# Kernel optimization log

Hardware: AMD Instinct MI355X
Metric: run time of the kernel (lower is better)

Reference implementation:

```python
import jax, jax.numpy as jnp
import numpy as np

B, S = 64, 100
N_EX, N_Q = 3000, 128
N_AT, N_IT = 1000, 1000
D_A = D_E = D_K = 128
GAMMA = 0.03


def _xavier(k, shape):
    lim = float(np.sqrt(6.0 / (shape[0] + shape[1])))
    return jax.random.uniform(k, shape, jnp.float32, -lim, lim)


def setup_inputs() -> dict:
    key = jax.random.key(0)
    ks = jax.random.split(key, 20)
    nq1 = N_Q + 1
    e_data = jax.random.randint(ks[0], (B, S), 0, N_EX, dtype=jnp.int32)
    a_data = jax.random.randint(ks[1], (B, S), 0, 2, dtype=jnp.int32)
    it_data = jax.random.randint(ks[2], (B, S), 0, N_IT, dtype=jnp.int32)
    at_data = jax.random.randint(ks[3], (B, S), 0, N_AT, dtype=jnp.int32)
    # binary Q-matrix with zeros replaced by gamma (as done in LPKT.__init__)
    q_bin = (jax.random.uniform(ks[4], (N_EX + 10, nq1)) < 0.05).astype(jnp.float32)
    q_matrix = jnp.where(q_bin > 0, 1.0, GAMMA)
    E_at = _xavier(ks[5], (N_AT + 10, D_K))
    E_it = _xavier(ks[6], (N_IT + 10, D_K))
    E_e = _xavier(ks[7], (N_EX + 10, D_E))
    h0 = _xavier(ks[8], (nq1, D_K))  # xavier-initialized initial skill state
    W1 = _xavier(ks[9], (D_A + D_E + D_K, D_K)); b1 = jnp.zeros(D_K, jnp.float32)
    W2 = _xavier(ks[10], (4 * D_K, D_K)); b2 = jnp.zeros(D_K, jnp.float32)
    W3 = _xavier(ks[11], (4 * D_K, D_K)); b3 = jnp.zeros(D_K, jnp.float32)
    W4 = _xavier(ks[12], (3 * D_K, D_K)); b4 = jnp.zeros(D_K, jnp.float32)
    W5 = _xavier(ks[13], (D_E + D_K, D_K)); b5 = jnp.zeros(D_K, jnp.float32)
    return dict(e_data=e_data, a_data=a_data, it_data=it_data, at_data=at_data,
                q_matrix=q_matrix, h0=h0, E_e=E_e, E_at=E_at, E_it=E_it,
                W1=W1, b1=b1, W2=W2, b2=b2, W3=W3, b3=b3, W4=W4, b4=b4, W5=W5, b5=b5)


def reference(e_data, a_data, it_data, at_data, q_matrix, h0, E_e, E_at, E_it,
              W1, b1, W2, b2, W3, b3, W4, b4, W5, b5):
    Bv, Sv = e_data.shape
    d_k = W2.shape[1]
    d_a = W1.shape[0] - E_e.shape[1] - d_k
    e_emb = E_e[e_data]            # (B,S,d_e)
    at_emb = E_at[at_data]         # (B,S,d_k)
    it_emb = E_it[it_data]         # (B,S,d_k)
    a_rep = jnp.broadcast_to(a_data.astype(jnp.float32)[..., None], (Bv, Sv, d_a))
    all_learning = jnp.concatenate([e_emb, at_emb, a_rep], 2) @ W1 + b1  # (B,S,d_k)
    q_all = q_matrix[e_data]       # (B,S,nq1)
    h_pre0 = jnp.broadcast_to(h0, (Bv,) + h0.shape)  # (B,nq1,d_k)
    q0 = q_all[:, 0]
    ht0 = jnp.einsum('bn,bnd->bd', q0, h_pre0) / q0.sum(1, keepdims=True)
    W4h, W4l, W4i = jnp.split(W4, 3, axis=0)

    def step(carry, x):
        learning_pre, h_pre, h_tilde_pre = carry
        q_e, q_next, it, learning, e_next = x
        feat = jnp.concatenate([learning_pre, it, learning, h_tilde_pre], 1)  # (B,4dk)
        lg = jnp.tanh(feat @ W2 + b2)
        gamma_l = jax.nn.sigmoid(feat @ W3 + b3)
        LG = gamma_l * (lg + 1.0) * 0.5                       # (B,d_k)
        LG_tilde = q_e[:, :, None] * LG[:, None, :]           # (B,nq1,d_k); dropout=eval identity
        gamma_f = jax.nn.sigmoid(jnp.einsum('bnd,df->bnf', h_pre, W4h)
                                 + (LG @ W4l + it @ W4i + b4)[:, None, :])
        h = LG_tilde + gamma_f * h_pre
        h_tilde = jnp.einsum('bn,bnd->bd', q_next, h) / q_next.sum(1, keepdims=True)
        y = jax.nn.sigmoid(jnp.concatenate([e_next, h_tilde], 1) @ W5 + b5).sum(1) / d_k
        return (learning, h, h_tilde), y

    xs = (jnp.swapaxes(q_all[:, :-1], 0, 1), jnp.swapaxes(q_all[:, 1:], 0, 1),
          jnp.swapaxes(it_emb[:, :-1], 0, 1), jnp.swapaxes(all_learning[:, :-1], 0, 1),
          jnp.swapaxes(e_emb[:, 1:], 0, 1))
    learning_pre0 = jnp.zeros((Bv, d_k), jnp.float32)
    _, ys = jax.lax.scan(step, (learning_pre0, h_pre0, ht0), xs)  # ys: (S-1,B)
    pred = jnp.zeros((Bv, Sv), jnp.float32).at[:, 1:].set(ys.T)
    return pred
```

## Files before the change

### kernel.cpp

```cpp
#include <hip/hip_runtime.h>
#include <hip/hip_fp16.h>
#include <math.h>


#define BB   64
#define SS   100
#define DK   128
#define NTH  512

#define OFF_PW1AB   0
#define OFF_PW23ABC 16384
#define OFF_PW4I    65536
#define OFF_PW5A    73728
#define OFF_PW23D   81920
#define OFF_PW4L    98304
#define OFF_PW5B    106496
#define OFF_AFRAG   114688
#define OFF_S1      122880
#define OFF_AL      123008
#define OFF_PRE     532608
#define OFF_HTV     2171008

typedef __attribute__((ext_vector_type(16))) float floatx16;
typedef __attribute__((ext_vector_type(8)))  short short8v;

__device__ __forceinline__ float frcp(float x) { return __builtin_amdgcn_rcpf(x); }
__device__ __forceinline__ float fsig(float x) { float t = __expf(-x); return frcp(1.0f + t); }
__device__ __forceinline__ float ftanh(float x) {
    x = fminf(20.0f, fmaxf(-20.0f, x));
    float t = __expf(-2.0f * x);
    return (1.0f - t) * frcp(1.0f + t);
}
__device__ __forceinline__ float rlf(float v, int s) {
    return __int_as_float(__builtin_amdgcn_readlane(__float_as_int(v), s));
}
__device__ __forceinline__ unsigned bfbits(float x) {
    unsigned u = __float_as_uint(x);
    return (u + 0x7fffu + ((u >> 16) & 1u)) >> 16;
}
__device__ __forceinline__ unsigned pack2(float a, float b) {
    return bfbits(a) | (bfbits(b) << 16);
}
__device__ __forceinline__ float blo(unsigned u) { return __uint_as_float(u << 16); }
__device__ __forceinline__ float bhi(unsigned u) { return __uint_as_float(u & 0xffff0000u); }

__device__ __forceinline__ void wg_barrier() {
    asm volatile("s_waitcnt lgkmcnt(0)" ::: "memory");
    __builtin_amdgcn_s_barrier();
    asm volatile("" ::: "memory");
}

__global__ void k0_prep(const float* __restrict__ W1, const float* __restrict__ W2,
                        const float* __restrict__ W3, const float* __restrict__ W4,
                        const float* __restrict__ W5, unsigned* __restrict__ ws) {
    int g = blockIdx.x * blockDim.x + threadIdx.x;
    if (g < 16384) {
        int s = g >> 7, d = g & 127;
        ws[OFF_PW1AB + g] = pack2(W1[(2*s)*DK + d], W1[(2*s+1)*DK + d]);
    } else if (g < 65536) {
        int i = g - 16384; int s = i >> 8, j = i & 255;
        const float* M = (j < 128) ? W2 : W3; int jj = j & 127;
        ws[g] = pack2(M[(2*s)*DK + jj], M[(2*s+1)*DK + jj]);
    } else if (g < 73728) {
        int i = g - 65536; int s = i >> 7, j = i & 127;
        ws[g] = pack2(W4[(256+2*s)*DK + j], W4[(257+2*s)*DK + j]);
    } else if (g < 81920) {
        int i = g - 73728; int s = i >> 7, j = i & 127;
        ws[g] = pack2(W5[(2*s)*DK + j], W5[(2*s+1)*DK + j]);
    } else if (g < 98304) {
        int i = g - 81920; int s = i & 31, j = (i >> 5) & 255, kh = i >> 13;
        int k0 = 64*kh + 2*s;
        const float* M = (j < 128) ? W2 : W3; int jj = j & 127;
        ws[g] = pack2(M[(384+k0)*DK + jj], M[(385+k0)*DK + jj]);
    } else if (g < 106496) {
        int i = g - 98304; int s = i & 15, j = (i >> 4) & 127, kq = i >> 11;
        int k0 = 32*kq + 2*s;
        ws[g] = pack2(W4[(128+k0)*DK + j], W4[(129+k0)*DK + j]);
    } else if (g < 114688) {
        int i = g - 106496; int s = i & 15, j = (i >> 4) & 127, kq = i >> 11;
        int k0 = 32*kq + 2*s;
        ws[g] = pack2(W5[(128+k0)*DK + j], W5[(129+k0)*DK + j]);
    } else if (g < 122880) {
        int i = g - 114688;
        int gg = i >> 11, kb = (i >> 8) & 7, ln = (i >> 2) & 63, c = i & 3;
        int m = ln & 31, hp = ln >> 5;
        int k0 = 16*kb + 8*hp + 2*c;
        ws[g] = pack2(W4[k0*DK + 32*gg + m], W4[(k0+1)*DK + 32*gg + m]);
    } else if (g < 123008) {
        int d = g - 122880;
        float z = 0.f;
        for (int k = 0; k < 128; k++) z += W1[(256+k)*DK + d];
        ws[g] = __float_as_uint(z);
    }
}

__global__ __launch_bounds__(128)
void k1_al(const int* __restrict__ e_data, const int* __restrict__ a_data,
           const int* __restrict__ at_data, const float* __restrict__ Ee,
           const float* __restrict__ Eat, const float* __restrict__ b1,
           unsigned* __restrict__ ws) {
    const int b = blockIdx.x, t0 = 4 * blockIdx.y, tid = threadIdx.x;
    __shared__ __align__(16) float s_f[4][256];
    #pragma unroll
    for (int r = 0; r < 8; r++) {
        int id = r * 128 + tid; int i = id >> 8, k = id & 255;
        int t = t0 + i; float v = 0.f;
        if (t <= 98) {
            int e  = e_data[b*SS + t];
            int at = at_data[b*SS + t];
            v = (k < 128) ? Ee[(size_t)e*DK + k] : Eat[(size_t)at*DK + (k-128)];
        }
        s_f[i][k] = v;
    }
    __syncthreads();
    float s1v = __uint_as_float(ws[OFF_S1 + tid]);
    float b1v = b1[tid];
    float z[4];
    #pragma unroll
    for (int i = 0; i < 4; i++) z[i] = 0.f;
    #pragma unroll 2
    for (int s = 0; s < 128; s++) {
        unsigned w = ws[OFF_PW1AB + s*128 + tid];
        float wl = blo(w), wh = bhi(w);
        #pragma unroll
        for (int i = 0; i < 4; i++) {
            float2 f = *(const float2*)&s_f[i][2*s];
            z[i] += f.x*wl + f.y*wh;
        }
    }
    __half* AL = (__half*)(ws + OFF_AL);
    #pragma unroll
    for (int i = 0; i < 4; i++) {
        int t = t0 + i;
        if (t <= 98) {
            float a = (float)a_data[b*SS + t];
            AL[(size_t)(b*SS + t)*DK + tid] = __float2half(z[i] + a*s1v + b1v);
        }
    }
}

__global__ __launch_bounds__(512)
void k2_pre(const int* __restrict__ e_data, const int* __restrict__ it_data,
            const float* __restrict__ Eit, const float* __restrict__ Ee,
            const float* __restrict__ b2, const float* __restrict__ b3,
            const float* __restrict__ b4, const float* __restrict__ b5,
            unsigned* __restrict__ ws) {
    const int b = blockIdx.x, t0 = 4 * blockIdx.y, tid = threadIdx.x;
    __shared__ __align__(16) float s_g[4][384];
    __shared__ __align__(16) float s_e[4][128];
    const __half* AL = (const __half*)(ws + OFF_AL);
    #pragma unroll
    for (int r = 0; r < 3; r++) {
        int id = r * 512 + tid; int i = id / 384; int k = id - 384*i;
        int t = t0 + i; float v = 0.f;
        if (t <= 98) {
            if (k < 128)      v = (t == 0) ? 0.f : (float)AL[(size_t)(b*SS + t - 1)*DK + k];
            else if (k < 256) v = Eit[(size_t)it_data[b*SS + t]*DK + (k - 128)];
            else              v = (float)AL[(size_t)(b*SS + t)*DK + (k - 256)];
        }
        s_g[i][k] = v;
    }
    {
        int id = tid; int i = id >> 7, k = id & 127;
        int t = t0 + i;
        s_e[i][k] = (t <= 98) ? Ee[(size_t)e_data[b*SS + t + 1]*DK + k] : 0.f;
    }
    __syncthreads();
    __half* PRE = (__half*)(ws + OFF_PRE);
    float z[4];
    #pragma unroll
    for (int i = 0; i < 4; i++) z[i] = 0.f;
    int col; float bb;
    if (tid < 256) {
        int j = tid;
        #pragma unroll 2
        for (int s = 0; s < 192; s++) {
            unsigned w = ws[OFF_PW23ABC + s*256 + j];
            float wl = blo(w), wh = bhi(w);
            #pragma unroll
            for (int i = 0; i < 4; i++) {
                float2 f = *(const float2*)&s_g[i][2*s];
                z[i] += f.x*wl + f.y*wh;
            }
        }
        col = j; bb = (j < 128) ? b2[j] : b3[j - 128];
    } else if (tid < 384) {
        int j = tid - 256;
        #pragma unroll 2
        for (int s = 0; s < 64; s++) {
            unsigned w = ws[OFF_PW4I + s*128 + j];
            float wl = blo(w), wh = bhi(w);
            #pragma unroll
            for (int i = 0; i < 4; i++) {
                float2 f = *(const float2*)&s_g[i][128 + 2*s];
                z[i] += f.x*wl + f.y*wh;
            }
        }
        col = 256 + j; bb = b4[j];
    } else {
        int j = tid - 384;
        #pragma unroll 2
        for (int s = 0; s < 64; s++) {
            unsigned w = ws[OFF_PW5A + s*128 + j];
            float wl = blo(w), wh = bhi(w);
            #pragma unroll
            for (int i = 0; i < 4; i++) {
                float2 f = *(const float2*)&s_e[i][2*s];
                z[i] += f.x*wl + f.y*wh;
            }
        }
        col = 384 + j; bb = b5[j];
    }
    #pragma unroll
    for (int i = 0; i < 4; i++) {
        int t = t0 + i;
        if (t <= 98) PRE[(size_t)(b*SS + t)*512 + col] = __float2half(z[i] + bb);
    }
}

__global__ __launch_bounds__(NTH, 2)
void lpkt_kernel(const int* __restrict__ e_data, const float* __restrict__ qm,
                 const float* __restrict__ h0, unsigned* __restrict__ ws)
{
    const int b    = blockIdx.x;
    const int tid  = threadIdx.x;
    const int lane = tid & 63;
    const int w    = tid >> 6;
    const int g    = w & 3;
    const int hh   = w >> 2;
    const int h5   = lane >> 5;
    const int l31  = lane & 31;
    const int j1   = tid & 255;
    const int kq4  = w & 3;
    const int j4   = ((w >> 2) << 6) + lane;

    __shared__ __align__(16) unsigned s_frag[8192];
    __shared__ __align__(16) float s_big[2 * 128 * 34];
    __shared__ __align__(16) float s_pre[2][512];
    __shared__ __align__(16) float s_htv[128];
    __shared__ __align__(16) float s_LG[128];
    __shared__ __align__(16) float s_h128[128];
    __shared__ __align__(16) float s_c[128];
    __shared__ __align__(16) float s_l128[2][128];
    __shared__ __align__(16) float s_red[512];
    __shared__ __align__(16) float s_redE[512];
    __shared__ __align__(16) float s_q[3][160];
    __shared__ int   s_ed[100];
    __shared__ float s_scal[1];

    uint4    afru[8];
    unsigned w23[32], w4l[16];
    float    hreg[2][16];

    #pragma unroll
    for (int kb = 0; kb < 8; kb++)
        afru[kb] = ((const uint4*)(ws + OFF_AFRAG))[g*512 + kb*64 + lane];
    #pragma unroll
    for (int s = 0; s < 32; s++) w23[s] = ws[OFF_PW23D + ((hh*256 + j1) << 5) + s];
    #pragma unroll
    for (int s = 0; s < 16; s++) w4l[s] = ws[OFF_PW4L + ((kq4*128 + j4) << 4) + s];

    const __half* PRE = (const __half*)(ws + OFF_PRE);
    __half*       HTV = (__half*)(ws + OFF_HTV);

    if (tid < 100) s_ed[tid] = e_data[b*SS + tid];
    if (tid < 160) { s_q[0][tid] = 0.f; s_q[1][tid] = 0.f; s_q[2][tid] = 0.f; }
    if (tid < 129) {
        s_q[0][tid] = qm[(size_t)e_data[b*SS + 0]*129 + tid];
        s_q[1][tid] = qm[(size_t)e_data[b*SS + 1]*129 + tid];
    }
    s_pre[0][tid] = __half2float(PRE[(size_t)(b*SS)*512 + tid]);
    float  q_pf   = (tid < 129) ? qm[(size_t)e_data[b*SS + 2]*129 + tid] : 0.f;
    __half pre_pf = PRE[(size_t)(b*SS + 1)*512 + tid];

    #pragma unroll
    for (int i = 0; i < 2; i++) {
        const int cb = 2*hh + i;
        const int n = 32*cb + l31;
        #pragma unroll
        for (int r = 0; r < 16; r++) {
            int d = 32*g + (r&3) + 8*(r>>2) + 4*h5;
            hreg[i][r] = h0[(size_t)n*DK + d];
        }
        #pragma unroll
        for (int q = 0; q < 4; q++) {
            int kb = 2*g + (q>>1);
            int lanep = l31 + ((q&1) << 5);
            int off = (((kb*4 + cb) << 10) + lanep*16 + (h5 << 3)) >> 2;
            uint2 pr = make_uint2(pack2(hreg[i][4*q],   hreg[i][4*q+1]),
                                  pack2(hreg[i][4*q+2], hreg[i][4*q+3]));
            *(uint2*)(s_frag + off) = pr;
        }
    }
    if (tid < 128) s_h128[tid] = h0[(size_t)128*DK + tid];
    __syncthreads();
    {
        if (w == 7) {
            float v = s_q[0][lane] + s_q[0][64+lane] + ((lane < 32) ? s_q[0][128+lane] : 0.f);
            #pragma unroll
            for (int m = 32; m > 0; m >>= 1) v += __shfl_xor(v, m);
            if (lane == 0) s_scal[0] = v;
        }
        float vv0[16];
        #pragma unroll
        for (int i = 0; i < 2; i++) {
            float qv = s_q[0][32*(2*hh + i) + l31];
            #pragma unroll
            for (int r = 0; r < 16; r++) {
                float p = qv * hreg[i][r];
                vv0[r] = i ? (vv0[r] + p) : p;
            }
        }
        #pragma unroll
        for (int r = 0; r < 16; r++) {
            int d = 32*g + (r&3) + 8*(r>>2) + 4*h5;
            s_big[(hh*128 + d)*34 + l31] = vv0[r];
        }
    }
    __syncthreads();
    if (tid < 128) {
        float a0 = 0.f, a1 = 0.f;
        #pragma unroll
        for (int jj = 0; jj < 16; jj++) {
            float2 x = *(const float2*)&s_big[tid*34 + 2*jj];
            float2 y = *(const float2*)&s_big[(128 + tid)*34 + 2*jj];
            a0 += x.x + x.y; a1 += y.x + y.y;
        }
        s_htv[tid] = (a0 + a1 + s_q[0][128]*s_h128[tid]) * frcp(s_scal[0]);
    }
    __syncthreads();

    for (int t = 0; t < SS - 1; t++) {
        const int pbp = t & 1;
        const float* qc = s_q[t % 3];
        const float* qn = s_q[(t + 1) % 3];

        if (t + 2 <= 99 && tid < 129) s_q[(t + 2) % 3][tid] = q_pf;
        if (t + 1 <= 98)              s_pre[1 - pbp][tid] = __half2float(pre_pf);
        if (t + 3 <= 99 && tid < 129) q_pf  = qm[(size_t)s_ed[t + 3]*129 + tid];
        if (t + 2 <= 98)              pre_pf = PRE[(size_t)(b*SS + t + 2)*512 + tid];
        if (w == 7) {
            float v = qn[lane] + qn[64 + lane] + ((lane < 32) ? qn[128 + lane] : 0.f);
            #pragma unroll
            for (int m = 32; m > 0; m >>= 1) v += __shfl_xor(v, m);
            if (lane == 0) s_scal[0] = v;
        }
        floatx16 am[2];
        #pragma unroll
        for (int i = 0; i < 2; i++) {
            const int cb = 2*hh + i;
            floatx16 a = (floatx16)(0.f);
            #pragma unroll
            for (int kb = 0; kb < 8; kb++) {
                short8v bf = *(const short8v*)((const char*)s_frag +
                               (((kb*4 + cb) << 10) + lane*16));
                a = __builtin_amdgcn_mfma_f32_32x32x16_bf16(
                        __builtin_bit_cast(short8v, afru[kb]), bf, a, 0, 0, 0);
            }
            am[i] = a;
        }
        {
            float part = 0.f;
            #pragma unroll
            for (int kbl = 0; kbl < 4; kbl++) {
                const int kb = 4*hh + kbl;
                const int kb0 = 16*kb + 8*h5;
                uint4 u = afru[kb];
                part += s_h128[kb0+0]*blo(u.x) + s_h128[kb0+1]*bhi(u.x);
                part += s_h128[kb0+2]*blo(u.y) + s_h128[kb0+3]*bhi(u.y);
                part += s_h128[kb0+4]*blo(u.z) + s_h128[kb0+5]*bhi(u.z);
                part += s_h128[kb0+6]*blo(u.w) + s_h128[kb0+7]*bhi(u.w);
            }
            part += __shfl_xor(part, 32);
            if (h5 == 0) s_l128[hh][32*g + l31] = part;
        }
        {
            float4 fv = ((const float4*)s_htv)[(hh << 4) + (l31 & 15)];
            float z0 = 0.f, z1 = 0.f, z2 = 0.f, z3 = 0.f;
            #pragma unroll
            for (int s = 0; s < 16; s++) {
                float a0 = rlf(fv.x, s), a1 = rlf(fv.y, s);
                float a2 = rlf(fv.z, s), a3 = rlf(fv.w, s);
                unsigned wA = w23[2*s], wB = w23[2*s+1];
                z0 += a0*blo(wA);  z1 += a1*bhi(wA);
                z2 += a2*blo(wB);  z3 += a3*bhi(wB);
            }
            s_red[(hh << 8) + j1] = (z0 + z1) + (z2 + z3);
        }
        wg_barrier();
        {
            const int m = 32*kq4 + l31;
            float z2v = s_red[m]       + s_red[256 + m] + s_pre[pbp][m];
            float z3v = s_red[128 + m] + s_red[384 + m] + s_pre[pbp][128 + m];
            float LGv = fsig(z3v) * (ftanh(z2v) + 1.f) * 0.5f;
            if (w < 4 && h5 == 0) s_LG[m] = LGv;
            float z0 = 0.f, z1 = 0.f, z2 = 0.f, z3 = 0.f;
            #pragma unroll
            for (int s = 0; s < 8; s++) {
                unsigned wA = w4l[2*s], wB = w4l[2*s+1];
                float a0 = rlf(LGv, 4*s+0), a1 = rlf(LGv, 4*s+1);
                float a2 = rlf(LGv, 4*s+2), a3 = rlf(LGv, 4*s+3);
                z0 += a0*blo(wA);  z1 += a1*bhi(wA);
                z2 += a2*blo(wB);  z3 += a3*bhi(wB);
            }
            s_redE[(kq4 << 7) + j4] = (z0 + z1) + (z2 + z3);
        }
        wg_barrier();
        if (tid < 128)
            s_c[tid] = s_redE[tid] + s_redE[128+tid] + s_redE[256+tid] + s_redE[384+tid]
                     + s_pre[pbp][256 + tid];
        wg_barrier();
        {
            float lgv[16], cvv[16], vv[16];
            const float4* LG4 = (const float4*)s_LG;
            const float4* C4  = (const float4*)s_c;
            #pragma unroll
            for (int u = 0; u < 4; u++) {
                float4 lg = LG4[8*g + 2*u + h5];
                float4 cc = C4 [8*g + 2*u + h5];
                lgv[4*u+0]=lg.x; lgv[4*u+1]=lg.y; lgv[4*u+2]=lg.z; lgv[4*u+3]=lg.w;
                cvv[4*u+0]=cc.x; cvv[4*u+1]=cc.y; cvv[4*u+2]=cc.z; cvv[4*u+3]=cc.w;
            }
            #pragma unroll
            for (int i = 0; i < 2; i++) {
                const int cb = 2*hh + i;
                const int n = 32*cb + l31;
                const float qcv = qc[n], qnv = qn[n];
                #pragma unroll
                for (int r = 0; r < 16; r++) {
                    float gg = fsig(am[i][r] + cvv[r]);
                    float hn = qcv*lgv[r] + gg*hreg[i][r];
                    hreg[i][r] = hn;
                    float p = qnv*hn;
                    vv[r] = i ? (vv[r] + p) : p;
                }
            }
            #pragma unroll
            for (int i = 0; i < 2; i++) {
                const int cb = 2*hh + i;
                #pragma unroll
                for (int q = 0; q < 4; q++) {
                    int kb = 2*g + (q>>1);
                    int lanep = l31 + ((q&1) << 5);
                    int off = (((kb*4 + cb) << 10) + lanep*16 + (h5 << 3)) >> 2;
                    uint2 pr = make_uint2(pack2(hreg[i][4*q],   hreg[i][4*q+1]),
                                          pack2(hreg[i][4*q+2], hreg[i][4*q+3]));
                    *(uint2*)(s_frag + off) = pr;
                }
            }
            #pragma unroll
            for (int r = 0; r < 16; r++) {
                int d = 32*g + (r&3) + 8*(r>>2) + 4*h5;
                s_big[(hh*128 + d)*34 + l31] = vv[r];
            }
            if (tid < 128) {
                float gg = fsig(s_l128[0][tid] + s_l128[1][tid] + s_c[tid]);
                s_h128[tid] = qc[128]*s_LG[tid] + gg*s_h128[tid];
            }
        }
        wg_barrier();
        if (tid < 128) {
            float a0 = 0.f, a1 = 0.f;
            #pragma unroll
            for (int jj = 0; jj < 16; jj++) {
                float2 x = *(const float2*)&s_big[tid*34 + 2*jj];
                float2 y = *(const float2*)&s_big[(128 + tid)*34 + 2*jj];
                a0 += x.x + x.y; a1 += y.x + y.y;
            }
            float htvv = (a0 + a1 + qn[128]*s_h128[tid]) * frcp(s_scal[0]);
            s_htv[tid] = htvv;
            HTV[((size_t)b*(SS-1) + t)*128 + tid] = __float2half(htvv);
        }
        wg_barrier();
    }
}

__global__ __launch_bounds__(128)
void k4_y(const float* __restrict__ W5, float* __restrict__ out,
          const unsigned* __restrict__ ws) {
    const int b = blockIdx.x, t = blockIdx.y, j = threadIdx.x;
    const __half* HTV = (const __half*)(ws + OFF_HTV);
    const __half* PRE = (const __half*)(ws + OFF_PRE);
    __shared__ float s_h[128];
    __shared__ float s_p[2];
    s_h[j] = __half2float(HTV[((size_t)b*(SS-1) + t)*128 + j]);
    __syncthreads();
    float z = __half2float(PRE[(size_t)(b*SS + t)*512 + 384 + j]);
    #pragma unroll 4
    for (int k = 0; k < 128; k++) z += s_h[k] * W5[(size_t)(128 + k)*DK + j];
    float v = fsig(z);
    #pragma unroll
    for (int m = 32; m > 0; m >>= 1) v += __shfl_xor(v, m);
    if ((j & 63) == 0) s_p[j >> 6] = v;
    __syncthreads();
    if (j == 0) {
        out[b*SS + t + 1] = (s_p[0] + s_p[1]) * (1.0f / 128.0f);
        if (t == 0) out[b*SS] = 0.f;
    }
}

extern "C" void kernel_launch(void* const* d_in, const int* in_sizes, int n_in,
                              void* d_out, int out_size, void* d_ws, size_t ws_size,
                              hipStream_t stream) {
    const int*   e_data  = (const int*)d_in[0];
    const int*   a_data  = (const int*)d_in[1];
    const int*   it_data = (const int*)d_in[2];
    const int*   at_data = (const int*)d_in[3];
    const float* qm  = (const float*)d_in[4];
    const float* h0  = (const float*)d_in[5];
    const float* Ee  = (const float*)d_in[6];
    const float* Eat = (const float*)d_in[7];
    const float* Eit = (const float*)d_in[8];
    const float* W1  = (const float*)d_in[9];
    const float* b1  = (const float*)d_in[10];
    const float* W2  = (const float*)d_in[11];
    const float* b2  = (const float*)d_in[12];
    const float* W3  = (const float*)d_in[13];
    const float* b3  = (const float*)d_in[14];
    const float* W4  = (const float*)d_in[15];
    const float* b4  = (const float*)d_in[16];
    const float* W5  = (const float*)d_in[17];
    const float* b5  = (const float*)d_in[18];
    float* out = (float*)d_out;
    unsigned* ws = (unsigned*)d_ws;

    k0_prep<<<dim3((123008 + 255) / 256), dim3(256), 0, stream>>>(W1, W2, W3, W4, W5, ws);
    k1_al<<<dim3(BB, 25), dim3(128), 0, stream>>>(e_data, a_data, at_data, Ee, Eat, b1, ws);
    k2_pre<<<dim3(BB, 25), dim3(512), 0, stream>>>(e_data, it_data, Eit, Ee, b2, b3, b4, b5, ws);
    lpkt_kernel<<<dim3(BB), dim3(NTH), 0, stream>>>(e_data, qm, h0, ws);
    k4_y<<<dim3(BB, SS - 1), dim3(128), 0, stream>>>(W5, out, ws);
}
```

Measured before the change: 805.6 us.

## Replace scalar readlane GEMVs in the recurrence with bf16 MFMA

The per-step h_tilde·W2/W3 projection and the LG·W4l projection in the sequential scan now run as 32x32x16 bf16 MFMA ops instead of scalar readlane FMA loops. The prep kernel repacks the weights into MFMA B-fragment layout, and the activations are packed to bf16 in LDS or gathered with ds_bpermute. This removes one barrier and the s_c reduction stage per step, shrinking serial latency in the recurrence. Only one column of each MFMA output is used, so most of the MFMA work is wasted, and the activations are now rounded to bf16.

```diff
diff --git a/kernel.cpp b/kernel.cpp
--- a/kernel.cpp
+++ b/kernel.cpp
@@ -14,7 +14,6 @@
 #define OFF_PW5A    73728
 #define OFF_PW23D   81920
 #define OFF_PW4L    98304
-#define OFF_PW5B    106496
 #define OFF_AFRAG   114688
 #define OFF_S1      122880
 #define OFF_AL      123008
@@ -30,9 +29,6 @@
     x = fminf(20.0f, fmaxf(-20.0f, x));
     float t = __expf(-2.0f * x);
     return (1.0f - t) * frcp(1.0f + t);
-}
-__device__ __forceinline__ float rlf(float v, int s) {
-    return __int_as_float(__builtin_amdgcn_readlane(__float_as_int(v), s));
 }
 __device__ __forceinline__ unsigned bfbits(float x) {
     unsigned u = __float_as_uint(x);
@@ -68,18 +64,19 @@
         int i = g - 73728; int s = i >> 7, j = i & 127;
         ws[g] = pack2(W5[(2*s)*DK + j], W5[(2*s+1)*DK + j]);
     } else if (g < 98304) {
-        int i = g - 81920; int s = i & 31, j = (i >> 5) & 255, kh = i >> 13;
-        int k0 = 64*kh + 2*s;
+        int i = g - 81920;
+        int q = i & 3, ln = (i >> 2) & 63, kb = (i >> 8) & 7, cw = i >> 11;
+        int k = 16*kb + 8*(ln >> 5) + 2*q;
+        int j = 32*cw + (ln & 31);
         const float* M = (j < 128) ? W2 : W3; int jj = j & 127;
-        ws[g] = pack2(M[(384+k0)*DK + jj], M[(385+k0)*DK + jj]);
+        ws[g] = pack2(M[(384+k)*DK + jj], M[(385+k)*DK + jj]);
     } else if (g < 106496) {
-        int i = g - 98304; int s = i & 15, j = (i >> 4) & 127, kq = i >> 11;
-        int k0 = 32*kq + 2*s;
-        ws[g] = pack2(W4[(128+k0)*DK + j], W4[(129+k0)*DK + j]);
+        int i = g - 98304;
+        int q = i & 3, ln = (i >> 2) & 63, kb = (i >> 8) & 7, cw = i >> 11;
+        int k = 16*kb + 8*(ln >> 5) + 2*q;
+        int j = 32*cw + (ln & 31);
+        ws[g] = pack2(W4[(128+k)*DK + j], W4[(129+k)*DK + j]);
     } else if (g < 114688) {
-        int i = g - 106496; int s = i & 15, j = (i >> 4) & 127, kq = i >> 11;
-        int k0 = 32*kq + 2*s;
-        ws[g] = pack2(W5[(128+k0)*DK + j], W5[(129+k0)*DK + j]);
     } else if (g < 122880) {
         int i = g - 114688;
         int gg = i >> 11, kb = (i >> 8) & 7, ln = (i >> 2) & 63, c = i & 3;
@@ -230,35 +227,34 @@
     const int hh   = w >> 2;
     const int h5   = lane >> 5;
     const int l31  = lane & 31;
-    const int j1   = tid & 255;
-    const int kq4  = w & 3;
-    const int j4   = ((w >> 2) << 6) + lane;
+    const int hf   = w >> 2;
+    const int cw3  = w & 3;
 
     __shared__ __align__(16) unsigned s_frag[8192];
     __shared__ __align__(16) float s_big[2 * 128 * 34];
     __shared__ __align__(16) float s_pre[2][512];
-    __shared__ __align__(16) float s_htv[128];
     __shared__ __align__(16) float s_LG[128];
     __shared__ __align__(16) float s_h128[128];
-    __shared__ __align__(16) float s_c[128];
     __shared__ __align__(16) float s_l128[2][128];
-    __shared__ __align__(16) float s_red[512];
-    __shared__ __align__(16) float s_redE[512];
+    __shared__ __align__(16) float s_red1[256];
+    __shared__ __align__(16) float s_redE[256];
+    __shared__ __align__(16) unsigned s_htvb[64];
     __shared__ __align__(16) float s_q[3][160];
     __shared__ int   s_ed[100];
     __shared__ float s_scal[1];
 
-    uint4    afru[8];
-    unsigned w23[32], w4l[16];
-    float    hreg[2][16];
+    uint4 afru[8], pw23b[8], pw4lb[4];
+    float hreg[2][16];
 
     #pragma unroll
     for (int kb = 0; kb < 8; kb++)
         afru[kb] = ((const uint4*)(ws + OFF_AFRAG))[g*512 + kb*64 + lane];
     #pragma unroll
-    for (int s = 0; s < 32; s++) w23[s] = ws[OFF_PW23D + ((hh*256 + j1) << 5) + s];
-    #pragma unroll
-    for (int s = 0; s < 16; s++) w4l[s] = ws[OFF_PW4L + ((kq4*128 + j4) << 4) + s];
+    for (int kb = 0; kb < 8; kb++)
+        pw23b[kb] = ((const uint4*)(ws + OFF_PW23D))[(w*8 + kb)*64 + lane];
+    #pragma unroll
+    for (int kbl = 0; kbl < 4; kbl++)
+        pw4lb[kbl] = ((const uint4*)(ws + OFF_PW4L))[((cw3*8 + hf*4 + kbl))*64 + lane];
 
     const __half* PRE = (const __half*)(ws + OFF_PRE);
     __half*       HTV = (__half*)(ws + OFF_HTV);
@@ -326,7 +322,9 @@
             float2 y = *(const float2*)&s_big[(128 + tid)*34 + 2*jj];
             a0 += x.x + x.y; a1 += y.x + y.y;
         }
-        s_htv[tid] = (a0 + a1 + s_q[0][128]*s_h128[tid]) * frcp(s_scal[0]);
+        float htvv = (a0 + a1 + s_q[0][128]*s_h128[tid]) * frcp(s_scal[0]);
+        float oth  = __shfl_xor(htvv, 1);
+        if (!(tid & 1)) s_htvb[tid >> 1] = pack2(htvv, oth);
     }
     __syncthreads();
 
@@ -344,6 +342,17 @@
             #pragma unroll
             for (int m = 32; m > 0; m >>= 1) v += __shfl_xor(v, m);
             if (lane == 0) s_scal[0] = v;
+        }
+        {
+            floatx16 p1 = (floatx16)(0.f);
+            #pragma unroll
+            for (int kb = 0; kb < 8; kb++) {
+                uint4 a1 = *(const uint4*)&s_htvb[kb*8 + 4*h5];
+                p1 = __builtin_amdgcn_mfma_f32_32x32x16_bf16(
+                        __builtin_bit_cast(short8v, a1),
+                        __builtin_bit_cast(short8v, pw23b[kb]), p1, 0, 0, 0);
+            }
+            if (h5 == 0) s_red1[w*32 + l31] = p1[0];
         }
         floatx16 am[2];
         #pragma unroll
@@ -374,52 +383,48 @@
             part += __shfl_xor(part, 32);
             if (h5 == 0) s_l128[hh][32*g + l31] = part;
         }
-        {
-            float4 fv = ((const float4*)s_htv)[(hh << 4) + (l31 & 15)];
-            float z0 = 0.f, z1 = 0.f, z2 = 0.f, z3 = 0.f;
-            #pragma unroll
-            for (int s = 0; s < 16; s++) {
-                float a0 = rlf(fv.x, s), a1 = rlf(fv.y, s);
-                float a2 = rlf(fv.z, s), a3 = rlf(fv.w, s);
-                unsigned wA = w23[2*s], wB = w23[2*s+1];
-                z0 += a0*blo(wA);  z1 += a1*bhi(wA);
-                z2 += a2*blo(wB);  z3 += a3*bhi(wB);
-            }
-            s_red[(hh << 8) + j1] = (z0 + z1) + (z2 + z3);
-        }
         wg_barrier();
         {
-            const int m = 32*kq4 + l31;
-            float z2v = s_red[m]       + s_red[256 + m] + s_pre[pbp][m];
-            float z3v = s_red[128 + m] + s_red[384 + m] + s_pre[pbp][128 + m];
+            const int m = 64*hf + lane;
+            float z2v = s_red1[m]       + s_pre[pbp][m];
+            float z3v = s_red1[128 + m] + s_pre[pbp][128 + m];
             float LGv = fsig(z3v) * (ftanh(z2v) + 1.f) * 0.5f;
-            if (w < 4 && h5 == 0) s_LG[m] = LGv;
-            float z0 = 0.f, z1 = 0.f, z2 = 0.f, z3 = 0.f;
-            #pragma unroll
-            for (int s = 0; s < 8; s++) {
-                unsigned wA = w4l[2*s], wB = w4l[2*s+1];
-                float a0 = rlf(LGv, 4*s+0), a1 = rlf(LGv, 4*s+1);
-                float a2 = rlf(LGv, 4*s+2), a3 = rlf(LGv, 4*s+3);
-                z0 += a0*blo(wA);  z1 += a1*bhi(wA);
-                z2 += a2*blo(wB);  z3 += a3*bhi(wB);
-            }
-            s_redE[(kq4 << 7) + j4] = (z0 + z1) + (z2 + z3);
-        }
-        wg_barrier();
-        if (tid < 128)
-            s_c[tid] = s_redE[tid] + s_redE[128+tid] + s_redE[256+tid] + s_redE[384+tid]
-                     + s_pre[pbp][256 + tid];
+            if (cw3 == 0) s_LG[m] = LGv;
+            float oth = __shfl_xor(LGv, 1);
+            float lo  = (lane & 1) ? oth : LGv;
+            float hi  = (lane & 1) ? LGv : oth;
+            int   pk  = (int)pack2(lo, hi);
+            floatx16 p3 = (floatx16)(0.f);
+            #pragma unroll
+            for (int kbl = 0; kbl < 4; kbl++) {
+                const int p0 = 8*kbl + 4*h5;
+                uint4 a3;
+                a3.x = (unsigned)__builtin_amdgcn_ds_bpermute(8*(p0+0), pk);
+                a3.y = (unsigned)__builtin_amdgcn_ds_bpermute(8*(p0+1), pk);
+                a3.z = (unsigned)__builtin_amdgcn_ds_bpermute(8*(p0+2), pk);
+                a3.w = (unsigned)__builtin_amdgcn_ds_bpermute(8*(p0+3), pk);
+                p3 = __builtin_amdgcn_mfma_f32_32x32x16_bf16(
+                        __builtin_bit_cast(short8v, a3),
+                        __builtin_bit_cast(short8v, pw4lb[kbl]), p3, 0, 0, 0);
+            }
+            if (h5 == 0) s_redE[hf*128 + 32*cw3 + l31] = p3[0];
+        }
         wg_barrier();
         {
             float lgv[16], cvv[16], vv[16];
             const float4* LG4 = (const float4*)s_LG;
-            const float4* C4  = (const float4*)s_c;
+            const float4* RE4 = (const float4*)s_redE;
+            const float4* PR4 = (const float4*)s_pre[pbp];
             #pragma unroll
             for (int u = 0; u < 4; u++) {
-                float4 lg = LG4[8*g + 2*u + h5];
-                float4 cc = C4 [8*g + 2*u + h5];
+                const int idx = 8*g + 2*u + h5;
+                float4 lg = LG4[idx];
+                float4 c0 = RE4[idx];
+                float4 c1 = RE4[32 + idx];
+                float4 pv = PR4[64 + idx];
                 lgv[4*u+0]=lg.x; lgv[4*u+1]=lg.y; lgv[4*u+2]=lg.z; lgv[4*u+3]=lg.w;
-                cvv[4*u+0]=cc.x; cvv[4*u+1]=cc.y; cvv[4*u+2]=cc.z; cvv[4*u+3]=cc.w;
+                cvv[4*u+0]=c0.x+c1.x+pv.x; cvv[4*u+1]=c0.y+c1.y+pv.y;
+                cvv[4*u+2]=c0.z+c1.z+pv.z; cvv[4*u+3]=c0.w+c1.w+pv.w;
             }
             #pragma unroll
             for (int i = 0; i < 2; i++) {
@@ -454,7 +459,8 @@
                 s_big[(hh*128 + d)*34 + l31] = vv[r];
             }
             if (tid < 128) {
-                float gg = fsig(s_l128[0][tid] + s_l128[1][tid] + s_c[tid]);
+                float c128 = s_redE[tid] + s_redE[128 + tid] + s_pre[pbp][256 + tid];
+                float gg = fsig(s_l128[0][tid] + s_l128[1][tid] + c128);
                 s_h128[tid] = qc[128]*s_LG[tid] + gg*s_h128[tid];
             }
         }
@@ -468,8 +474,9 @@
                 a0 += x.x + x.y; a1 += y.x + y.y;
             }
             float htvv = (a0 + a1 + qn[128]*s_h128[tid]) * frcp(s_scal[0]);
-            s_htv[tid] = htvv;
             HTV[((size_t)b*(SS-1) + t)*128 + tid] = __float2half(htvv);
+            float oth = __shfl_xor(htvv, 1);
+            if (!(tid & 1)) s_htvb[tid >> 1] = pack2(htvv, oth);
         }
         wg_barrier();
     }
```

Result: faster. 676.7 us (-16.0%).
